# Kernel optimization log

Hardware: AMD Instinct MI355X
Metric: run time of the kernel (lower is better)

The kernel has to match this reference:

```python
import jax, jax.numpy as jnp
import numpy as np

LAMDA = 0.1  # matches init_kwargs lamda

T_AVG = 8192
N_STEPS = 2048


def setup_inputs() -> dict:
    key = jax.random.key(0)
    k1, k2 = jax.random.split(key)
    n = N_STEPS * T_AVG
    return {
        "input": jax.random.normal(k1, (n,), dtype=jnp.float32),
        "target": jax.random.normal(k2, (n,), dtype=jnp.float32),
        "Taverage": T_AVG,
        "nSteps": N_STEPS,
    }


def reference(input, target, Taverage, nSteps):
    T = int(Taverage)
    N = int(nSteps)
    # nested loop == sum of squared diffs between consecutive length-T blocks
    x = input[: N * T].reshape(N, T)          # [N, T]
    d = x[:-1] - x[1:]                        # [N-1, T]
    sum_accum = jnp.sum(d * d)
    nom_l1 = jnp.where(N != 1, LAMDA * jnp.sqrt(sum_accum), jnp.float32(0.0))
    mse = jnp.mean((input - target) ** 2)     # MSELoss(size_average=True)
    return mse + nom_l1
```

## Files before the change

kernel.cpp:

```cpp
#include <hip/hip_runtime.h>


#define LAMDA 0.1
#define BLOCK 256
#define GRID 2048

__global__ __launch_bounds__(BLOCK, 4) void cyclic_reduce_kernel(
    const float4* __restrict__ in4,
    const float4* __restrict__ tg4,
    const int* __restrict__ pT,
    const int* __restrict__ pN,
    long long n,
    double* __restrict__ m_part,
    double* __restrict__ d_part)
{
    const int T = pT[0];
    const int N = pN[0];
    const int n4 = (int)(n >> 2);
    const int t4 = T >> 2;
    const long long limit = (N > 1) ? (long long)(N - 1) * (long long)T : 0;
    const int limit4 = (int)(limit >> 2);

    float mse_acc = 0.0f;
    float dif_acc = 0.0f;

    const int nth  = (int)gridDim.x * BLOCK;
    const int gtid = (int)blockIdx.x * BLOCK + (int)threadIdx.x;

    int i = gtid;
    for (; i + 3 * nth < limit4; i += 4 * nth) {
        const int i1 = i + nth, i2 = i + 2 * nth, i3 = i + 3 * nth;

        float4 a0 = in4[i];        float4 c0 = in4[i + t4];
        float4 a1 = in4[i1];       float4 c1 = in4[i1 + t4];
        float4 a2 = in4[i2];       float4 c2 = in4[i2 + t4];
        float4 a3 = in4[i3];       float4 c3 = in4[i3 + t4];
        float4 b0 = tg4[i];        float4 b1 = tg4[i1];
        float4 b2 = tg4[i2];       float4 b3 = tg4[i3];

        float e0, e1, e2, e3, d0, d1, d2, d3;
        e0 = a0.x - b0.x; e1 = a0.y - b0.y; e2 = a0.z - b0.z; e3 = a0.w - b0.w;
        mse_acc += e0 * e0 + e1 * e1 + e2 * e2 + e3 * e3;
        d0 = a0.x - c0.x; d1 = a0.y - c0.y; d2 = a0.z - c0.z; d3 = a0.w - c0.w;
        dif_acc += d0 * d0 + d1 * d1 + d2 * d2 + d3 * d3;

        e0 = a1.x - b1.x; e1 = a1.y - b1.y; e2 = a1.z - b1.z; e3 = a1.w - b1.w;
        mse_acc += e0 * e0 + e1 * e1 + e2 * e2 + e3 * e3;
        d0 = a1.x - c1.x; d1 = a1.y - c1.y; d2 = a1.z - c1.z; d3 = a1.w - c1.w;
        dif_acc += d0 * d0 + d1 * d1 + d2 * d2 + d3 * d3;

        e0 = a2.x - b2.x; e1 = a2.y - b2.y; e2 = a2.z - b2.z; e3 = a2.w - b2.w;
        mse_acc += e0 * e0 + e1 * e1 + e2 * e2 + e3 * e3;
        d0 = a2.x - c2.x; d1 = a2.y - c2.y; d2 = a2.z - c2.z; d3 = a2.w - c2.w;
        dif_acc += d0 * d0 + d1 * d1 + d2 * d2 + d3 * d3;

        e0 = a3.x - b3.x; e1 = a3.y - b3.y; e2 = a3.z - b3.z; e3 = a3.w - b3.w;
        mse_acc += e0 * e0 + e1 * e1 + e2 * e2 + e3 * e3;
        d0 = a3.x - c3.x; d1 = a3.y - c3.y; d2 = a3.z - c3.z; d3 = a3.w - c3.w;
        dif_acc += d0 * d0 + d1 * d1 + d2 * d2 + d3 * d3;
    }
    for (; i < limit4; i += nth) {
        float4 a = in4[i];
        float4 c = in4[i + t4];
        float4 b = tg4[i];
        float e0 = a.x - b.x, e1 = a.y - b.y, e2 = a.z - b.z, e3 = a.w - b.w;
        mse_acc += e0 * e0 + e1 * e1 + e2 * e2 + e3 * e3;
        float d0 = a.x - c.x, d1 = a.y - c.y, d2 = a.z - c.z, d3 = a.w - c.w;
        dif_acc += d0 * d0 + d1 * d1 + d2 * d2 + d3 * d3;
    }

    for (int k = limit4 + gtid; k < n4; k += nth) {
        float4 a = in4[k];
        float4 b = tg4[k];
        float e0 = a.x - b.x, e1 = a.y - b.y, e2 = a.z - b.z, e3 = a.w - b.w;
        mse_acc += e0 * e0 + e1 * e1 + e2 * e2 + e3 * e3;
    }

    {
        const float* in = (const float*)in4;
        const float* tg = (const float*)tg4;
        long long idx = ((long long)n4 << 2) + gtid;
        if (idx < n) {
            float e = in[idx] - tg[idx];
            mse_acc += e * e;
        }
        long long didx = ((long long)limit4 << 2) + gtid;
        if (didx < limit) {
            float d = in[didx] - in[didx + T];
            dif_acc += d * d;
        }
    }

    #pragma unroll
    for (int off = 32; off > 0; off >>= 1) {
        mse_acc += __shfl_down(mse_acc, off, 64);
        dif_acc += __shfl_down(dif_acc, off, 64);
    }
    __shared__ float s_m[4], s_d[4];
    const int wave = threadIdx.x >> 6;
    if ((threadIdx.x & 63) == 0) { s_m[wave] = mse_acc; s_d[wave] = dif_acc; }
    __syncthreads();
    if (threadIdx.x == 0) {
        m_part[blockIdx.x] = (double)s_m[0] + (double)s_m[1] + (double)s_m[2] + (double)s_m[3];
        d_part[blockIdx.x] = (double)s_d[0] + (double)s_d[1] + (double)s_d[2] + (double)s_d[3];
    }
}

#define FBLOCK 1024

__global__ __launch_bounds__(FBLOCK) void cyclic_finalize_kernel(
    const double* __restrict__ m_part,
    const double* __restrict__ d_part,
    const int* __restrict__ pN,
    float* __restrict__ out,
    long long n,
    int nparts)
{
    double m = 0.0, d = 0.0;
    for (int i = threadIdx.x; i < nparts; i += FBLOCK) {
        m += m_part[i];
        d += d_part[i];
    }
    #pragma unroll
    for (int off = 32; off > 0; off >>= 1) {
        m += __shfl_down(m, off, 64);
        d += __shfl_down(d, off, 64);
    }
    __shared__ double f_m[FBLOCK / 64], f_d[FBLOCK / 64];
    const int wave = threadIdx.x >> 6;
    if ((threadIdx.x & 63) == 0) { f_m[wave] = m; f_d[wave] = d; }
    __syncthreads();
    if (threadIdx.x == 0) {
        double mt = 0.0, dt = 0.0;
        #pragma unroll
        for (int w = 0; w < FBLOCK / 64; ++w) { mt += f_m[w]; dt += f_d[w]; }
        double mse = mt / (double)n;
        double nom = (pN[0] != 1) ? (LAMDA * sqrt(dt)) : 0.0;
        out[0] = (float)(mse + nom);
    }
}

extern "C" void kernel_launch(void* const* d_in, const int* in_sizes, int n_in,
                              void* d_out, int out_size, void* d_ws, size_t ws_size,
                              hipStream_t stream) {
    const float* input  = (const float*)d_in[0];
    const float* target = (const float*)d_in[1];
    const int*   pT     = (const int*)d_in[2];
    const int*   pN     = (const int*)d_in[3];
    float* out = (float*)d_out;

    const long long n = (long long)in_sizes[0];

    double* m_part = (double*)d_ws;
    double* d_part = m_part + GRID;

    cyclic_reduce_kernel<<<GRID, BLOCK, 0, stream>>>(
        (const float4*)input, (const float4*)target, pT, pN, n, m_part, d_part);

    cyclic_finalize_kernel<<<1, FBLOCK, 0, stream>>>(m_part, d_part, pN, out, n, GRID);
}
```

Measured before the change: 150.1 us.

## Tile reduction by row segments so each input row is loaded once

Adds a fast path that gives each block a column chunk across 8 consecutive rows of the input matrix. Each thread loads those 8 rows plus one halo row and the matching target values into registers, then computes both the MSE and the consecutive-row difference terms from them. Before, each input element was read twice (as row i and as row i+1), so this cuts global traffic and issues all loads up front for more memory-level parallelism. The fast path runs only when T, N and the grid size divide exactly; otherwise the original grid-stride loop is used. Holding 17 float4 values per thread raises register pressure.

```diff
diff --git a/kernel.cpp b/kernel.cpp
--- a/kernel.cpp
+++ b/kernel.cpp
@@ -4,6 +4,7 @@
 #define LAMDA 0.1
 #define BLOCK 256
 #define GRID 2048
+#define RSEG 8
 
 __global__ __launch_bounds__(BLOCK, 4) void cyclic_reduce_kernel(
     const float4* __restrict__ in4,
@@ -24,70 +25,114 @@
     float mse_acc = 0.0f;
     float dif_acc = 0.0f;
 
-    const int nth  = (int)gridDim.x * BLOCK;
-    const int gtid = (int)blockIdx.x * BLOCK + (int)threadIdx.x;
-
-    int i = gtid;
-    for (; i + 3 * nth < limit4; i += 4 * nth) {
-        const int i1 = i + nth, i2 = i + 2 * nth, i3 = i + 3 * nth;
-
-        float4 a0 = in4[i];        float4 c0 = in4[i + t4];
-        float4 a1 = in4[i1];       float4 c1 = in4[i1 + t4];
-        float4 a2 = in4[i2];       float4 c2 = in4[i2 + t4];
-        float4 a3 = in4[i3];       float4 c3 = in4[i3 + t4];
-        float4 b0 = tg4[i];        float4 b1 = tg4[i1];
-        float4 b2 = tg4[i2];       float4 b3 = tg4[i3];
-
-        float e0, e1, e2, e3, d0, d1, d2, d3;
-        e0 = a0.x - b0.x; e1 = a0.y - b0.y; e2 = a0.z - b0.z; e3 = a0.w - b0.w;
-        mse_acc += e0 * e0 + e1 * e1 + e2 * e2 + e3 * e3;
-        d0 = a0.x - c0.x; d1 = a0.y - c0.y; d2 = a0.z - c0.z; d3 = a0.w - c0.w;
-        dif_acc += d0 * d0 + d1 * d1 + d2 * d2 + d3 * d3;
-
-        e0 = a1.x - b1.x; e1 = a1.y - b1.y; e2 = a1.z - b1.z; e3 = a1.w - b1.w;
-        mse_acc += e0 * e0 + e1 * e1 + e2 * e2 + e3 * e3;
-        d0 = a1.x - c1.x; d1 = a1.y - c1.y; d2 = a1.z - c1.z; d3 = a1.w - c1.w;
-        dif_acc += d0 * d0 + d1 * d1 + d2 * d2 + d3 * d3;
-
-        e0 = a2.x - b2.x; e1 = a2.y - b2.y; e2 = a2.z - b2.z; e3 = a2.w - b2.w;
-        mse_acc += e0 * e0 + e1 * e1 + e2 * e2 + e3 * e3;
-        d0 = a2.x - c2.x; d1 = a2.y - c2.y; d2 = a2.z - c2.z; d3 = a2.w - c2.w;
-        dif_acc += d0 * d0 + d1 * d1 + d2 * d2 + d3 * d3;
-
-        e0 = a3.x - b3.x; e1 = a3.y - b3.y; e2 = a3.z - b3.z; e3 = a3.w - b3.w;
-        mse_acc += e0 * e0 + e1 * e1 + e2 * e2 + e3 * e3;
-        d0 = a3.x - c3.x; d1 = a3.y - c3.y; d2 = a3.z - c3.z; d3 = a3.w - c3.w;
-        dif_acc += d0 * d0 + d1 * d1 + d2 * d2 + d3 * d3;
-    }
-    for (; i < limit4; i += nth) {
-        float4 a = in4[i];
-        float4 c = in4[i + t4];
-        float4 b = tg4[i];
-        float e0 = a.x - b.x, e1 = a.y - b.y, e2 = a.z - b.z, e3 = a.w - b.w;
-        mse_acc += e0 * e0 + e1 * e1 + e2 * e2 + e3 * e3;
-        float d0 = a.x - c.x, d1 = a.y - c.y, d2 = a.z - c.z, d3 = a.w - c.w;
-        dif_acc += d0 * d0 + d1 * d1 + d2 * d2 + d3 * d3;
-    }
-
-    for (int k = limit4 + gtid; k < n4; k += nth) {
-        float4 a = in4[k];
-        float4 b = tg4[k];
-        float e0 = a.x - b.x, e1 = a.y - b.y, e2 = a.z - b.z, e3 = a.w - b.w;
-        mse_acc += e0 * e0 + e1 * e1 + e2 * e2 + e3 * e3;
-    }
-
-    {
-        const float* in = (const float*)in4;
-        const float* tg = (const float*)tg4;
-        long long idx = ((long long)n4 << 2) + gtid;
-        if (idx < n) {
-            float e = in[idx] - tg[idx];
-            mse_acc += e * e;
-        }
-        long long didx = ((long long)limit4 << 2) + gtid;
-        if (didx < limit) {
-            float d = in[didx] - in[didx + T];
-            dif_acc += d * d;
+    const int colchunks = (T % 4 == 0) ? (t4 / BLOCK) : 0;
+    bool fast = (colchunks > 0) && (t4 % BLOCK == 0)
+             && ((long long)N * (long long)T == n)
+             && ((int)gridDim.x % colchunks == 0);
+    int rowsegs = 0;
+    if (fast) {
+        rowsegs = (int)gridDim.x / colchunks;
+        fast = (rowsegs > 0) && (N % rowsegs == 0) && (N / rowsegs == RSEG);
+    }
+
+    if (fast) {
+        const int seg      = (int)blockIdx.x;
+        const int colchunk = seg % colchunks;
+        const int rowseg   = seg / colchunks;
+        const int row0     = rowseg * RSEG;
+        const int col4     = colchunk * BLOCK + (int)threadIdx.x;
+        const float4* px = in4 + (long long)row0 * t4 + col4;
+        const float4* pt = tg4 + (long long)row0 * t4 + col4;
+
+        const bool has9 = (row0 + RSEG < N);
+        const int  ofs9 = has9 ? RSEG * t4 : (RSEG - 1) * t4;
+
+        float4 x[RSEG + 1];
+        float4 b[RSEG];
+        #pragma unroll
+        for (int k = 0; k < RSEG; ++k) x[k] = px[k * t4];
+        x[RSEG] = px[ofs9];
+        #pragma unroll
+        for (int k = 0; k < RSEG; ++k) b[k] = pt[k * t4];
+
+        #pragma unroll
+        for (int k = 0; k < RSEG; ++k) {
+            float e0 = x[k].x - b[k].x, e1 = x[k].y - b[k].y;
+            float e2 = x[k].z - b[k].z, e3 = x[k].w - b[k].w;
+            mse_acc += e0 * e0 + e1 * e1 + e2 * e2 + e3 * e3;
+        }
+        #pragma unroll
+        for (int k = 0; k < RSEG - 1; ++k) {
+            float d0 = x[k].x - x[k + 1].x, d1 = x[k].y - x[k + 1].y;
+            float d2 = x[k].z - x[k + 1].z, d3 = x[k].w - x[k + 1].w;
+            dif_acc += d0 * d0 + d1 * d1 + d2 * d2 + d3 * d3;
+        }
+        {
+            float d0 = x[RSEG - 1].x - x[RSEG].x, d1 = x[RSEG - 1].y - x[RSEG].y;
+            float d2 = x[RSEG - 1].z - x[RSEG].z, d3 = x[RSEG - 1].w - x[RSEG].w;
+            float dd = d0 * d0 + d1 * d1 + d2 * d2 + d3 * d3;
+            dif_acc += has9 ? dd : 0.0f;
+        }
+    } else {
+        const int nth  = (int)gridDim.x * BLOCK;
+        const int gtid = (int)blockIdx.x * BLOCK + (int)threadIdx.x;
+
+        int i = gtid;
+        for (; i + 3 * nth < limit4; i += 4 * nth) {
+            const int i1 = i + nth, i2 = i + 2 * nth, i3 = i + 3 * nth;
+            float4 a0 = in4[i];        float4 c0 = in4[i + t4];
+            float4 a1 = in4[i1];       float4 c1 = in4[i1 + t4];
+            float4 a2 = in4[i2];       float4 c2 = in4[i2 + t4];
+            float4 a3 = in4[i3];       float4 c3 = in4[i3 + t4];
+            float4 b0 = tg4[i];        float4 b1 = tg4[i1];
+            float4 b2 = tg4[i2];       float4 b3 = tg4[i3];
+
+            float e0, e1, e2, e3, d0, d1, d2, d3;
+            e0 = a0.x - b0.x; e1 = a0.y - b0.y; e2 = a0.z - b0.z; e3 = a0.w - b0.w;
+            mse_acc += e0 * e0 + e1 * e1 + e2 * e2 + e3 * e3;
+            d0 = a0.x - c0.x; d1 = a0.y - c0.y; d2 = a0.z - c0.z; d3 = a0.w - c0.w;
+            dif_acc += d0 * d0 + d1 * d1 + d2 * d2 + d3 * d3;
+            e0 = a1.x - b1.x; e1 = a1.y - b1.y; e2 = a1.z - b1.z; e3 = a1.w - b1.w;
+            mse_acc += e0 * e0 + e1 * e1 + e2 * e2 + e3 * e3;
+            d0 = a1.x - c1.x; d1 = a1.y - c1.y; d2 = a1.z - c1.z; d3 = a1.w - c1.w;
+            dif_acc += d0 * d0 + d1 * d1 + d2 * d2 + d3 * d3;
+            e0 = a2.x - b2.x; e1 = a2.y - b2.y; e2 = a2.z - b2.z; e3 = a2.w - b2.w;
+            mse_acc += e0 * e0 + e1 * e1 + e2 * e2 + e3 * e3;
+            d0 = a2.x - c2.x; d1 = a2.y - c2.y; d2 = a2.z - c2.z; d3 = a2.w - c2.w;
+            dif_acc += d0 * d0 + d1 * d1 + d2 * d2 + d3 * d3;
+            e0 = a3.x - b3.x; e1 = a3.y - b3.y; e2 = a3.z - b3.z; e3 = a3.w - b3.w;
+            mse_acc += e0 * e0 + e1 * e1 + e2 * e2 + e3 * e3;
+            d0 = a3.x - c3.x; d1 = a3.y - c3.y; d2 = a3.z - c3.z; d3 = a3.w - c3.w;
+            dif_acc += d0 * d0 + d1 * d1 + d2 * d2 + d3 * d3;
+        }
+        for (; i < limit4; i += nth) {
+            float4 a = in4[i];
+            float4 c = in4[i + t4];
+            float4 b = tg4[i];
+            float e0 = a.x - b.x, e1 = a.y - b.y, e2 = a.z - b.z, e3 = a.w - b.w;
+            mse_acc += e0 * e0 + e1 * e1 + e2 * e2 + e3 * e3;
+            float d0 = a.x - c.x, d1 = a.y - c.y, d2 = a.z - c.z, d3 = a.w - c.w;
+            dif_acc += d0 * d0 + d1 * d1 + d2 * d2 + d3 * d3;
+        }
+        for (int k = limit4 + gtid; k < n4; k += nth) {
+            float4 a = in4[k];
+            float4 b = tg4[k];
+            float e0 = a.x - b.x, e1 = a.y - b.y, e2 = a.z - b.z, e3 = a.w - b.w;
+            mse_acc += e0 * e0 + e1 * e1 + e2 * e2 + e3 * e3;
+        }
+        {
+            const float* in = (const float*)in4;
+            const float* tg = (const float*)tg4;
+            long long idx = ((long long)n4 << 2) + gtid;
+            if (idx < n) {
+                float e = in[idx] - tg[idx];
+                mse_acc += e * e;
+            }
+            long long didx = ((long long)limit4 << 2) + gtid;
+            if (didx < limit) {
+                float d = in[didx] - in[didx + T];
+                dif_acc += d * d;
+            }
         }
     }
 
```

New measurement: 150.0 us. No clear change (-0.1%).
